# Optimization experiments

Measured on AMD Instinct MI355X. Metric: run time of the kernel, lower is better.

The kernel has to match this reference:

```python
import jax, jax.numpy as jnp
import numpy as np
import math

NUM_BUCKETS = 32
MAX_DISTANCE = 128
N_HEADS = 16
D_KV = 64


def _relative_position_bucket(relative_position, num_buckets=NUM_BUCKETS, max_distance=MAX_DISTANCE):
    # bidirectional (encoder) variant
    num_buckets //= 2
    relative_buckets = (relative_position > 0).astype(jnp.int32) * num_buckets
    rp = jnp.abs(relative_position)
    max_exact = num_buckets // 2
    is_small = rp < max_exact
    rp_large = max_exact + (
        jnp.log(jnp.maximum(rp, 1).astype(jnp.float32) / max_exact)
        / math.log(max_distance / max_exact)
        * (num_buckets - max_exact)
    ).astype(jnp.int32)
    rp_large = jnp.minimum(rp_large, num_buckets - 1)
    return relative_buckets + jnp.where(is_small, rp, rp_large)


def compute_bias(rel_bias, q_len, k_len):
    ctx = jnp.arange(q_len)[:, None]
    mem = jnp.arange(k_len)[None, :]
    buckets = _relative_position_bucket(mem - ctx)          # [q, k]
    values = rel_bias[buckets]                               # [q, k, h]
    return jnp.transpose(values, (2, 0, 1))[None]            # [1, h, q, k]


def setup_inputs() -> dict:
    key = jax.random.key(0)
    ks = jax.random.split(key, 6)
    d_model, inner = 1024, N_HEADS * D_KV
    s = 0.02
    return {
        "hidden_states": jax.random.normal(ks[0], (2, 2048, d_model), jnp.float32),
        "Wq": jax.random.normal(ks[1], (d_model, inner), jnp.float32) * s,
        "Wk": jax.random.normal(ks[2], (d_model, inner), jnp.float32) * s,
        "Wv": jax.random.normal(ks[3], (d_model, inner), jnp.float32) * s,
        "Wo": jax.random.normal(ks[4], (inner, d_model), jnp.float32) * s,
        "rel_bias": jax.random.normal(ks[5], (NUM_BUCKETS, N_HEADS), jnp.float32) * s,
    }


def reference(hidden_states, Wq, Wk, Wv, Wo, rel_bias):
    B, S, D = hidden_states.shape

    def split_heads(x):  # [B,S,inner] -> [B,H,S,dk]
        return x.reshape(B, S, N_HEADS, D_KV).transpose(0, 2, 1, 3)

    q = split_heads(hidden_states @ Wq)
    k = split_heads(hidden_states @ Wk)
    v = split_heads(hidden_states @ Wv)

    # T5 does NOT scale by 1/sqrt(d_kv)
    scores = jnp.einsum("bhqd,bhkd->bhqk", q, k)
    scores = scores + compute_bias(rel_bias, S, S)
    attn = jax.nn.softmax(scores, axis=-1)
    ctx = jnp.einsum("bhqk,bhkd->bhqd", attn, v)
    ctx = ctx.transpose(0, 2, 1, 3).reshape(B, S, N_HEADS * D_KV)
    return ctx @ Wo
```

## Files before the change

### kernel.cpp

```cpp
#include <hip/hip_runtime.h>
#include <hip/hip_bf16.h>

typedef __bf16 bf16x8 __attribute__((ext_vector_type(8)));
typedef __bf16 bf16x4 __attribute__((ext_vector_type(4)));
typedef float floatx4 __attribute__((ext_vector_type(4)));
typedef float floatx16 __attribute__((ext_vector_type(16)));
using bf16 = __hip_bfloat16;

#define S_    2048
#define NHEAD 16
#define LOG2E 1.4426950408889634f

__device__ __forceinline__ void load_lds16(const bf16* g, void* lds) {
  __builtin_amdgcn_global_load_lds((const __attribute__((address_space(1))) void*)g,
                                   (__attribute__((address_space(3))) void*)lds, 16, 0, 0);
}

__global__ void prep_kernel(const float* __restrict__ hidden,
                            const float* __restrict__ wq, const float* __restrict__ wk,
                            const float* __restrict__ wv, const float* __restrict__ wo,
                            const float* __restrict__ rel_bias,
                            bf16* __restrict__ hbf, bf16* __restrict__ wt_qkv,
                            bf16* __restrict__ wt_o, float* __restrict__ tab) {
  __shared__ bf16 tile[32][33];
  int bid = blockIdx.x;
  if (bid < 4096) {
    int i = (bid * 256 + threadIdx.x) * 4;
    float4 v = *(const float4*)(hidden + i);
    bf16 o[4] = {__float2bfloat16(v.x), __float2bfloat16(v.y),
                 __float2bfloat16(v.z), __float2bfloat16(v.w)};
    *(uint2*)(hbf + i) = *(const uint2*)o;
  } else if (bid < 8192) {
    int r = bid - 4096;
    int mat = r >> 10;
    int rem = r & 1023;
    int n0 = (rem & 31) * 32, k0 = (rem >> 5) * 32;
    int tx = threadIdx.x & 31, ty = threadIdx.x >> 5;
    const float* src = (mat == 0) ? wq : (mat == 1) ? wk : (mat == 2) ? wv : wo;
    bf16* dst = (mat == 3) ? wt_o : wt_qkv + mat * 1024 * 1024;
#pragma unroll
    for (int j = 0; j < 32; j += 8)
      tile[ty + j][tx] = __float2bfloat16(src[(k0 + ty + j) * 1024 + n0 + tx]);
    __syncthreads();
#pragma unroll
    for (int j = 0; j < 32; j += 8)
      dst[(n0 + ty + j) * 1024 + k0 + tx] = tile[tx][ty + j];
  } else {
    int idx = (bid - 8192) * 256 + threadIdx.x;
    int h = idx >> 12, j = idx & 4095;
    int delta = j - 2048;
    int rb = (delta > 0) ? 16 : 0;
    int rpa = delta < 0 ? -delta : delta;
    int bsmall;
    if (rpa < 8) {
      bsmall = rpa;
    } else {
      int lg = 25 - __clz(rpa * rpa);
      bsmall = 8 + lg;
      if (bsmall > 15) bsmall = 15;
    }
    tab[idx] = rel_bias[(rb + bsmall) * 16 + h] * LOG2E;
  }
}

__global__ __launch_bounds__(256) void gemm_qkv_kernel(const bf16* __restrict__ A,
                                                       const bf16* __restrict__ Bt,
                                                       bf16* __restrict__ qh,
                                                       bf16* __restrict__ kf,
                                                       bf16* __restrict__ vf) {
  const int K = 1024;
  __shared__ bf16 As[128 * 32];
  __shared__ bf16 Bs[128 * 32];
  int t = threadIdx.x;
  int m0 = blockIdx.y * 128, n0 = blockIdx.x * 128;
  int w = t >> 6, lane = t & 63, ln = lane & 15, quad = lane >> 4;
  int wr = w >> 1, wc = w & 1;
  floatx4 acc[4][4];
  floatx4 zero = {0.f, 0.f, 0.f, 0.f};
#pragma unroll
  for (int i = 0; i < 4; i++)
#pragma unroll
    for (int j = 0; j < 4; j++) acc[i][j] = zero;

  int r = t >> 2, c = (t & 3) * 8;
  const bf16* Ag = A + (long)(m0 + r) * K + c;
  const bf16* Bg = Bt + (long)(n0 + r) * K + c;
  char* ldsA0 = (char*)As + w * 1024;
  char* ldsA1 = ldsA0 + 4096;
  char* ldsB0 = (char*)Bs + w * 1024;
  char* ldsB1 = ldsB0 + 4096;

  for (int k0 = 0; k0 < K; k0 += 32) {
    load_lds16(Ag + k0, ldsA0);
    load_lds16(Ag + (long)64 * K + k0, ldsA1);
    load_lds16(Bg + k0, ldsB0);
    load_lds16(Bg + (long)64 * K + k0, ldsB1);
    __syncthreads();
    bf16x8 af[4], bfv[4];
#pragma unroll
    for (int i = 0; i < 4; i++)
      af[i] = *(const bf16x8*)&As[(wr * 64 + i * 16 + ln) * 32 + quad * 8];
#pragma unroll
    for (int j = 0; j < 4; j++)
      bfv[j] = *(const bf16x8*)&Bs[(wc * 64 + j * 16 + ln) * 32 + quad * 8];
#pragma unroll
    for (int i = 0; i < 4; i++)
#pragma unroll
      for (int j = 0; j < 4; j++)
        acc[i][j] = __builtin_amdgcn_mfma_f32_16x16x32_bf16(af[i], bfv[j], acc[i][j], 0, 0, 0);
    __syncthreads();
  }

  int nb = n0 + wc * 64;
  int type = nb >> 10, h = (nb >> 6) & 15;
  int b = (m0 >> 11);
  int sl0 = (m0 & 2047) + wr * 64;
  long bhbase = (long)((b * 16 + h)) * 131072;

  if (type == 0) {
#pragma unroll
    for (int i = 0; i < 4; i++)
#pragma unroll
      for (int j = 0; j < 4; j++) {
        int d = j * 16 + ln;
#pragma unroll
        for (int rr = 0; rr < 4; rr++) {
          int s = sl0 + i * 16 + quad * 4 + rr;
          qh[bhbase + (long)s * 64 + d] = __float2bfloat16(acc[i][j][rr]);
        }
      }
  } else if (type == 1) {
#pragma unroll
    for (int i = 0; i < 4; i++)
#pragma unroll
      for (int j = 0; j < 4; j++) {
        long base = bhbase + sl0 * 64 + (i >> 1) * 2048 + j * 512 + (ln >> 3) * 256 +
                    (i & 1) * 128 + quad * 32 + (ln & 7);
#pragma unroll
        for (int rr = 0; rr < 4; rr++)
          kf[base + rr * 8] = __float2bfloat16(acc[i][j][rr]);
      }
  } else {
#pragma unroll
    for (int i = 0; i < 4; i++)
#pragma unroll
      for (int j = 0; j < 4; j++) {
        long off = sl0 * 64 + i * 1024 + (j >> 1) * 512 + (quad >> 1) * 256 +
                   ((j & 1) * 16 + ln) * 8 + (quad & 1) * 4;
        bf16x4 pk = {(__bf16)acc[i][j][0], (__bf16)acc[i][j][1],
                     (__bf16)acc[i][j][2], (__bf16)acc[i][j][3]};
        *(bf16x4*)(vf + bhbase + off) = pk;
      }
  }
}

__global__ __launch_bounds__(128, 2) void attn_kernel(const bf16* __restrict__ qh,
                                                      const bf16* __restrict__ kf,
                                                      const bf16* __restrict__ vf,
                                                      const float* __restrict__ btab,
                                                      bf16* __restrict__ ctx) {
  __shared__ char KV[2][16384];
  int t = threadIdx.x, w = t >> 6, lane = t & 63;
  int l31 = lane & 31, h5 = lane >> 5;
  int bh = blockIdx.x, b = bh >> 4, h = bh & 15;
  int qw = blockIdx.y * 64 + w * 32;

  const bf16* qbase = qh + (long)bh * S_ * 64;
  const bf16* kfb = kf + (long)bh * S_ * 64;
  const bf16* vfb = vf + (long)bh * S_ * 64;
  const float* bt = btab + h * 4096;

  bf16x8 Qf[4];
#pragma unroll
  for (int ds = 0; ds < 4; ds++)
    Qf[ds] = *(const bf16x8*)(qbase + (long)(qw + l31) * 64 + ds * 16 + h5 * 8);

  float cneg = bt[0], cpos = bt[4095];
  float l_acc = 0.f;
  floatx16 zf = {0.f, 0.f, 0.f, 0.f, 0.f, 0.f, 0.f, 0.f,
                 0.f, 0.f, 0.f, 0.f, 0.f, 0.f, 0.f, 0.f};
  floatx16 o0 = zf, o1 = zf;

  {
    const bf16* kg = kfb + t * 8;
    const bf16* vg = vfb + t * 8;
#pragma unroll
    for (int c = 0; c < 4; c++) {
      load_lds16(kg + c * 1024, KV[0] + c * 2048 + w * 1024);
      load_lds16(vg + c * 1024, KV[0] + 8192 + c * 2048 + w * 1024);
    }
  }

  int pb = 0;
  for (int k0 = 0; k0 < S_; k0 += 64) {
    __syncthreads();
    int kn = k0 + 64;
    if (kn < S_) {
      const bf16* kg = kfb + kn * 64 + t * 8;
      const bf16* vg = vfb + kn * 64 + t * 8;
      char* nb_ = KV[pb ^ 1];
#pragma unroll
      for (int c = 0; c < 4; c++) {
        load_lds16(kg + c * 1024, nb_ + c * 2048 + w * 1024);
        load_lds16(vg + c * 1024, nb_ + 8192 + c * 2048 + w * 1024);
      }
    }

    const char* bK = KV[pb];
    const char* bV = KV[pb] + 8192;

    floatx16 st0 = zf, st1 = zf;
#pragma unroll
    for (int ds = 0; ds < 4; ds++) {
      bf16x8 Kf0 = *(const bf16x8*)(bK + ds * 1024 + lane * 16);
      st0 = __builtin_amdgcn_mfma_f32_32x32x16_bf16(Kf0, Qf[ds], st0, 0, 0, 0);
    }
#pragma unroll
    for (int ds = 0; ds < 4; ds++) {
      bf16x8 Kf1 = *(const bf16x8*)(bK + 4096 + ds * 1024 + lane * 16);
      st1 = __builtin_amdgcn_mfma_f32_32x32x16_bf16(Kf1, Qf[ds], st1, 0, 0, 0);
    }

    bf16x8 Af[4];
    bool near = (k0 > qw - 192) && (k0 < qw + 160);
#pragma unroll
    for (int s = 0; s < 2; s++) {
      const floatx16 stv = s ? st1 : st0;
      float p[16];
      if (near) {
        int kb = k0 + s * 32 + 4 * h5 - (qw + l31) + 2048;
#pragma unroll
        for (int r = 0; r < 16; r++)
          p[r] = __builtin_amdgcn_exp2f(
              fmaf(stv[r], LOG2E, bt[kb + (r & 3) + 8 * (r >> 2)]));
      } else {
        float cb = (k0 > qw) ? cpos : cneg;
#pragma unroll
        for (int r = 0; r < 16; r++)
          p[r] = __builtin_amdgcn_exp2f(fmaf(stv[r], LOG2E, cb));
      }
      float a0 = (p[0] + p[1]) + (p[2] + p[3]);
      float a1 = (p[4] + p[5]) + (p[6] + p[7]);
      float a2 = (p[8] + p[9]) + (p[10] + p[11]);
      float a3 = (p[12] + p[13]) + (p[14] + p[15]);
      l_acc += (a0 + a1) + (a2 + a3);

      unsigned d[8];
#pragma unroll
      for (int i = 0; i < 8; i++)
        asm("v_cvt_pk_bf16_f32 %0, %1, %2" : "=v"(d[i]) : "v"(p[2 * i]), "v"(p[2 * i + 1]));
      unsigned w0 = d[0], w2 = d[2];
      asm("v_permlane32_swap_b32 %0, %1" : "+v"(w0), "+v"(w2));
      unsigned w1 = d[1], w3 = d[3];
      asm("v_permlane32_swap_b32 %0, %1" : "+v"(w1), "+v"(w3));
      unsigned w4 = d[4], w6 = d[6];
      asm("v_permlane32_swap_b32 %0, %1" : "+v"(w4), "+v"(w6));
      unsigned w5 = d[5], w7 = d[7];
      asm("v_permlane32_swap_b32 %0, %1" : "+v"(w5), "+v"(w7));
      union { unsigned u[4]; bf16x8 v; } a0u, a1u;
      a0u.u[0] = w0; a0u.u[1] = w1; a0u.u[2] = w2; a0u.u[3] = w3;
      a1u.u[0] = w4; a1u.u[1] = w5; a1u.u[2] = w6; a1u.u[3] = w7;
      Af[s * 2 + 0] = a0u.v;
      Af[s * 2 + 1] = a1u.v;
    }

#pragma unroll
    for (int tt = 0; tt < 4; tt++) {
      bf16x8 Vf0 = *(const bf16x8*)(bV + tt * 2048 + lane * 16);
      bf16x8 Vf1 = *(const bf16x8*)(bV + tt * 2048 + 1024 + lane * 16);
      o0 = __builtin_amdgcn_mfma_f32_32x32x16_bf16(Af[tt], Vf0, o0, 0, 0, 0);
      o1 = __builtin_amdgcn_mfma_f32_32x32x16_bf16(Af[tt], Vf1, o1, 0, 0, 0);
    }

    pb ^= 1;
  }

  l_acc += __shfl_xor(l_acc, 32);
  float linv = 1.0f / l_acc;
#pragma unroll
  for (int r = 0; r < 16; r++) {
    int qrow = (r & 3) + 8 * (r >> 2) + 4 * h5;
    float lv = __shfl(linv, qrow);
    int q = qw + qrow;
    long base = (long)(b * S_ + q) * 1024 + h * 64 + l31;
    ctx[base] = __float2bfloat16(o0[r] * lv);
    ctx[base + 32] = __float2bfloat16(o1[r] * lv);
  }
}

__global__ __launch_bounds__(256) void gemm_bt_kernel(const bf16* __restrict__ A,
                                                      const bf16* __restrict__ Bt,
                                                      float* __restrict__ C,
                                                      int M, int N, int K) {
  __shared__ bf16 As[128 * 32];
  __shared__ bf16 Bs[128 * 32];
  int t = threadIdx.x;
  int m0 = blockIdx.y * 128, n0 = blockIdx.x * 128;
  int w = t >> 6, lane = t & 63, ln = lane & 15, quad = lane >> 4;
  int wr = w >> 1, wc = w & 1;
  floatx4 acc[4][4];
  floatx4 zero = {0.f, 0.f, 0.f, 0.f};
#pragma unroll
  for (int i = 0; i < 4; i++)
#pragma unroll
    for (int j = 0; j < 4; j++) acc[i][j] = zero;

  int r = t >> 2, c = (t & 3) * 8;
  const bf16* Ag = A + (long)(m0 + r) * K + c;
  const bf16* Bg = Bt + (long)(n0 + r) * K + c;
  char* ldsA0 = (char*)As + w * 1024;
  char* ldsA1 = ldsA0 + 4096;
  char* ldsB0 = (char*)Bs + w * 1024;
  char* ldsB1 = ldsB0 + 4096;

  for (int k0 = 0; k0 < K; k0 += 32) {
    load_lds16(Ag + k0, ldsA0);
    load_lds16(Ag + (long)64 * K + k0, ldsA1);
    load_lds16(Bg + k0, ldsB0);
    load_lds16(Bg + (long)64 * K + k0, ldsB1);
    __syncthreads();
    bf16x8 af[4], bfv[4];
#pragma unroll
    for (int i = 0; i < 4; i++)
      af[i] = *(const bf16x8*)&As[(wr * 64 + i * 16 + ln) * 32 + quad * 8];
#pragma unroll
    for (int j = 0; j < 4; j++)
      bfv[j] = *(const bf16x8*)&Bs[(wc * 64 + j * 16 + ln) * 32 + quad * 8];
#pragma unroll
    for (int i = 0; i < 4; i++)
#pragma unroll
      for (int j = 0; j < 4; j++)
        acc[i][j] = __builtin_amdgcn_mfma_f32_16x16x32_bf16(af[i], bfv[j], acc[i][j], 0, 0, 0);
    __syncthreads();
  }

#pragma unroll
  for (int i = 0; i < 4; i++)
#pragma unroll
    for (int j = 0; j < 4; j++)
#pragma unroll
      for (int rr = 0; rr < 4; rr++)
        C[(long)(m0 + wr * 64 + i * 16 + quad * 4 + rr) * N + n0 + wc * 64 + j * 16 + ln] =
            acc[i][j][rr];
}

extern "C" void kernel_launch(void* const* d_in, const int* in_sizes, int n_in,
                              void* d_out, int out_size, void* d_ws, size_t ws_size,
                              hipStream_t stream) {
  (void)in_sizes; (void)n_in; (void)out_size; (void)ws_size;
  const float* hidden   = (const float*)d_in[0];
  const float* Wq       = (const float*)d_in[1];
  const float* Wk       = (const float*)d_in[2];
  const float* Wv       = (const float*)d_in[3];
  const float* Wo       = (const float*)d_in[4];
  const float* rel_bias = (const float*)d_in[5];

  char* ws = (char*)d_ws;
  bf16*  hbf    = (bf16*)(ws + 0);
  bf16*  wt_qkv = (bf16*)(ws + 8388608);
  bf16*  wt_o   = (bf16*)(ws + 14680064);
  float* btab   = (float*)(ws + 16777216);
  bf16*  qh     = (bf16*)(ws + 17039360);
  bf16*  kf     = (bf16*)(ws + 25427968);
  bf16*  vf     = (bf16*)(ws + 33816576);
  bf16*  ctx    = (bf16*)(ws + 42205184);

  prep_kernel<<<dim3(8448), dim3(256), 0, stream>>>(hidden, Wq, Wk, Wv, Wo, rel_bias,
                                                    hbf, wt_qkv, wt_o, btab);
  gemm_qkv_kernel<<<dim3(24, 32), dim3(256), 0, stream>>>(hbf, wt_qkv, qh, kf, vf);
  attn_kernel<<<dim3(32, 32), dim3(128), 0, stream>>>(qh, kf, vf, btab, ctx);
  gemm_bt_kernel<<<dim3(8, 32), dim3(256), 0, stream>>>(ctx, wt_o, (float*)d_out, 4096, 1024, 1024);
}
```

Before: 201.8 us.

## Stream K/V fragments directly from global into registers, dropping LDS staging

The attention kernel no longer stages K/V tiles through double-buffered LDS with block-wide barriers. Each wave now loads its K/V MFMA fragments straight from global memory into registers, using two register sets to prefetch the next 32-key chunk while the current one is computed. The block grows to 4 waves over 128 query rows, the grid order is swapped so blocks of the same head sit together, and s_setprio is raised around the MFMA groups. This removes the barriers and LDS traffic, but every wave re-reads K/V from global/L2 and register pressure rises.

```diff
diff --git a/kernel.cpp b/kernel.cpp
--- a/kernel.cpp
+++ b/kernel.cpp
@@ -154,21 +154,86 @@
   }
 }
 
-__global__ __launch_bounds__(128, 2) void attn_kernel(const bf16* __restrict__ qh,
+#define LOADKV(Kr, Vr, kk)                                        \
+  {                                                               \
+    const bf16* kp = kfb + (kk) * 64 + loff;                      \
+    const bf16* vp = vfb + (kk) * 64 + loff;                      \
+    Kr[0] = *(const bf16x8*)(kp);                                 \
+    Kr[1] = *(const bf16x8*)(kp + 512);                           \
+    Kr[2] = *(const bf16x8*)(kp + 1024);                          \
+    Kr[3] = *(const bf16x8*)(kp + 1536);                          \
+    Vr[0] = *(const bf16x8*)(vp);                                 \
+    Vr[1] = *(const bf16x8*)(vp + 512);                           \
+    Vr[2] = *(const bf16x8*)(vp + 1024);                          \
+    Vr[3] = *(const bf16x8*)(vp + 1536);                          \
+  }
+
+#define COMPUTE(Kr, Vr, kk)                                                       \
+  {                                                                               \
+    floatx16 st = zf;                                                             \
+    __builtin_amdgcn_s_setprio(1);                                                \
+    st = __builtin_amdgcn_mfma_f32_32x32x16_bf16(Kr[0], Qf[0], st, 0, 0, 0);      \
+    st = __builtin_amdgcn_mfma_f32_32x32x16_bf16(Kr[1], Qf[1], st, 0, 0, 0);      \
+    st = __builtin_amdgcn_mfma_f32_32x32x16_bf16(Kr[2], Qf[2], st, 0, 0, 0);      \
+    st = __builtin_amdgcn_mfma_f32_32x32x16_bf16(Kr[3], Qf[3], st, 0, 0, 0);      \
+    __builtin_amdgcn_s_setprio(0);                                                \
+    float p[16];                                                                  \
+    bool near = ((kk) > qw - 160) && ((kk) < qw + 160);                           \
+    if (near) {                                                                   \
+      int kb = (kk) + 4 * h5 - (qw + l31) + 2048;                                 \
+      _Pragma("unroll")                                                           \
+      for (int r = 0; r < 16; r++)                                                \
+        p[r] = __builtin_amdgcn_exp2f(                                            \
+            fmaf(st[r], LOG2E, bt[kb + (r & 3) + 8 * (r >> 2)]));                 \
+    } else {                                                                      \
+      float cb = ((kk) > qw) ? cpos : cneg;                                       \
+      _Pragma("unroll")                                                           \
+      for (int r = 0; r < 16; r++)                                                \
+        p[r] = __builtin_amdgcn_exp2f(fmaf(st[r], LOG2E, cb));                    \
+    }                                                                             \
+    float a0 = (p[0] + p[1]) + (p[2] + p[3]);                                     \
+    float a1 = (p[4] + p[5]) + (p[6] + p[7]);                                     \
+    float a2 = (p[8] + p[9]) + (p[10] + p[11]);                                   \
+    float a3 = (p[12] + p[13]) + (p[14] + p[15]);                                 \
+    l_acc += (a0 + a1) + (a2 + a3);                                               \
+    unsigned d[8];                                                                \
+    _Pragma("unroll")                                                             \
+    for (int i = 0; i < 8; i++)                                                   \
+      asm("v_cvt_pk_bf16_f32 %0, %1, %2" : "=v"(d[i]) : "v"(p[2*i]), "v"(p[2*i+1])); \
+    unsigned w0 = d[0], w2 = d[2];                                                \
+    asm("v_permlane32_swap_b32 %0, %1" : "+v"(w0), "+v"(w2));                     \
+    unsigned w1 = d[1], w3 = d[3];                                                \
+    asm("v_permlane32_swap_b32 %0, %1" : "+v"(w1), "+v"(w3));                     \
+    unsigned w4 = d[4], w6 = d[6];                                                \
+    asm("v_permlane32_swap_b32 %0, %1" : "+v"(w4), "+v"(w6));                     \
+    unsigned w5 = d[5], w7 = d[7];                                                \
+    asm("v_permlane32_swap_b32 %0, %1" : "+v"(w5), "+v"(w7));                     \
+    union { unsigned u[4]; bf16x8 v; } a0u, a1u;                                  \
+    a0u.u[0] = w0; a0u.u[1] = w1; a0u.u[2] = w2; a0u.u[3] = w3;                   \
+    a1u.u[0] = w4; a1u.u[1] = w5; a1u.u[2] = w6; a1u.u[3] = w7;                   \
+    __builtin_amdgcn_s_setprio(1);                                                \
+    o0 = __builtin_amdgcn_mfma_f32_32x32x16_bf16(a0u.v, Vr[0], o0, 0, 0, 0);      \
+    o1 = __builtin_amdgcn_mfma_f32_32x32x16_bf16(a0u.v, Vr[1], o1, 0, 0, 0);      \
+    o0 = __builtin_amdgcn_mfma_f32_32x32x16_bf16(a1u.v, Vr[2], o0, 0, 0, 0);      \
+    o1 = __builtin_amdgcn_mfma_f32_32x32x16_bf16(a1u.v, Vr[3], o1, 0, 0, 0);      \
+    __builtin_amdgcn_s_setprio(0);                                                \
+  }
+
+__global__ __launch_bounds__(256, 2) void attn_kernel(const bf16* __restrict__ qh,
                                                       const bf16* __restrict__ kf,
                                                       const bf16* __restrict__ vf,
                                                       const float* __restrict__ btab,
                                                       bf16* __restrict__ ctx) {
-  __shared__ char KV[2][16384];
   int t = threadIdx.x, w = t >> 6, lane = t & 63;
   int l31 = lane & 31, h5 = lane >> 5;
-  int bh = blockIdx.x, b = bh >> 4, h = bh & 15;
-  int qw = blockIdx.y * 64 + w * 32;
+  int bh = blockIdx.y, b = bh >> 4, h = bh & 15;
+  int qw = blockIdx.x * 128 + w * 32;
 
   const bf16* qbase = qh + (long)bh * S_ * 64;
   const bf16* kfb = kf + (long)bh * S_ * 64;
   const bf16* vfb = vf + (long)bh * S_ * 64;
   const float* bt = btab + h * 4096;
+  int loff = h5 * 256 + l31 * 8;
 
   bf16x8 Qf[4];
 #pragma unroll
@@ -181,98 +246,15 @@
                  0.f, 0.f, 0.f, 0.f, 0.f, 0.f, 0.f, 0.f};
   floatx16 o0 = zf, o1 = zf;
 
-  {
-    const bf16* kg = kfb + t * 8;
-    const bf16* vg = vfb + t * 8;
-#pragma unroll
-    for (int c = 0; c < 4; c++) {
-      load_lds16(kg + c * 1024, KV[0] + c * 2048 + w * 1024);
-      load_lds16(vg + c * 1024, KV[0] + 8192 + c * 2048 + w * 1024);
-    }
-  }
-
-  int pb = 0;
+  bf16x8 Ka[4], Va[4], Kb[4], Vb[4];
+  LOADKV(Ka, Va, 0);
+  LOADKV(Kb, Vb, 32);
+
   for (int k0 = 0; k0 < S_; k0 += 64) {
-    __syncthreads();
-    int kn = k0 + 64;
-    if (kn < S_) {
-      const bf16* kg = kfb + kn * 64 + t * 8;
-      const bf16* vg = vfb + kn * 64 + t * 8;
-      char* nb_ = KV[pb ^ 1];
-#pragma unroll
-      for (int c = 0; c < 4; c++) {
-        load_lds16(kg + c * 1024, nb_ + c * 2048 + w * 1024);
-        load_lds16(vg + c * 1024, nb_ + 8192 + c * 2048 + w * 1024);
-      }
-    }
-
-    const char* bK = KV[pb];
-    const char* bV = KV[pb] + 8192;
-
-    floatx16 st0 = zf, st1 = zf;
-#pragma unroll
-    for (int ds = 0; ds < 4; ds++) {
-      bf16x8 Kf0 = *(const bf16x8*)(bK + ds * 1024 + lane * 16);
-      st0 = __builtin_amdgcn_mfma_f32_32x32x16_bf16(Kf0, Qf[ds], st0, 0, 0, 0);
-    }
-#pragma unroll
-    for (int ds = 0; ds < 4; ds++) {
-      bf16x8 Kf1 = *(const bf16x8*)(bK + 4096 + ds * 1024 + lane * 16);
-      st1 = __builtin_amdgcn_mfma_f32_32x32x16_bf16(Kf1, Qf[ds], st1, 0, 0, 0);
-    }
-
-    bf16x8 Af[4];
-    bool near = (k0 > qw - 192) && (k0 < qw + 160);
-#pragma unroll
-    for (int s = 0; s < 2; s++) {
-      const floatx16 stv = s ? st1 : st0;
-      float p[16];
-      if (near) {
-        int kb = k0 + s * 32 + 4 * h5 - (qw + l31) + 2048;
-#pragma unroll
-        for (int r = 0; r < 16; r++)
-          p[r] = __builtin_amdgcn_exp2f(
-              fmaf(stv[r], LOG2E, bt[kb + (r & 3) + 8 * (r >> 2)]));
-      } else {
-        float cb = (k0 > qw) ? cpos : cneg;
-#pragma unroll
-        for (int r = 0; r < 16; r++)
-          p[r] = __builtin_amdgcn_exp2f(fmaf(stv[r], LOG2E, cb));
-      }
-      float a0 = (p[0] + p[1]) + (p[2] + p[3]);
-      float a1 = (p[4] + p[5]) + (p[6] + p[7]);
-      float a2 = (p[8] + p[9]) + (p[10] + p[11]);
-      float a3 = (p[12] + p[13]) + (p[14] + p[15]);
-      l_acc += (a0 + a1) + (a2 + a3);
-
-      unsigned d[8];
-#pragma unroll
-      for (int i = 0; i < 8; i++)
-        asm("v_cvt_pk_bf16_f32 %0, %1, %2" : "=v"(d[i]) : "v"(p[2 * i]), "v"(p[2 * i + 1]));
-      unsigned w0 = d[0], w2 = d[2];
-      asm("v_permlane32_swap_b32 %0, %1" : "+v"(w0), "+v"(w2));
-      unsigned w1 = d[1], w3 = d[3];
-      asm("v_permlane32_swap_b32 %0, %1" : "+v"(w1), "+v"(w3));
-      unsigned w4 = d[4], w6 = d[6];
-      asm("v_permlane32_swap_b32 %0, %1" : "+v"(w4), "+v"(w6));
-      unsigned w5 = d[5], w7 = d[7];
-      asm("v_permlane32_swap_b32 %0, %1" : "+v"(w5), "+v"(w7));
-      union { unsigned u[4]; bf16x8 v; } a0u, a1u;
-      a0u.u[0] = w0; a0u.u[1] = w1; a0u.u[2] = w2; a0u.u[3] = w3;
-      a1u.u[0] = w4; a1u.u[1] = w5; a1u.u[2] = w6; a1u.u[3] = w7;
-      Af[s * 2 + 0] = a0u.v;
-      Af[s * 2 + 1] = a1u.v;
-    }
-
-#pragma unroll
-    for (int tt = 0; tt < 4; tt++) {
-      bf16x8 Vf0 = *(const bf16x8*)(bV + tt * 2048 + lane * 16);
-      bf16x8 Vf1 = *(const bf16x8*)(bV + tt * 2048 + 1024 + lane * 16);
-      o0 = __builtin_amdgcn_mfma_f32_32x32x16_bf16(Af[tt], Vf0, o0, 0, 0, 0);
-      o1 = __builtin_amdgcn_mfma_f32_32x32x16_bf16(Af[tt], Vf1, o1, 0, 0, 0);
-    }
-
-    pb ^= 1;
+    COMPUTE(Ka, Va, k0);
+    if (k0 + 64 < S_) LOADKV(Ka, Va, k0 + 64);
+    COMPUTE(Kb, Vb, k0 + 32);
+    if (k0 + 96 < S_) LOADKV(Kb, Vb, k0 + 96);
   }
 
   l_acc += __shfl_xor(l_acc, 32);
@@ -368,6 +350,6 @@
   prep_kernel<<<dim3(8448), dim3(256), 0, stream>>>(hidden, Wq, Wk, Wv, Wo, rel_bias,
                                                     hbf, wt_qkv, wt_o, btab);
   gemm_qkv_kernel<<<dim3(24, 32), dim3(256), 0, stream>>>(hbf, wt_qkv, qh, kf, vf);
-  attn_kernel<<<dim3(32, 32), dim3(128), 0, stream>>>(qh, kf, vf, btab, ctx);
+  attn_kernel<<<dim3(16, 32), dim3(256), 0, stream>>>(qh, kf, vf, btab, ctx);
   gemm_bt_kernel<<<dim3(8, 32), dim3(256), 0, stream>>>(ctx, wt_o, (float*)d_out, 4096, 1024, 1024);
 }
```

New measurement: 195.2 us. 3.3% less time.

## Split attention KV range across warps, load K/V directly to registers

Applied to the files above, without the earlier changes.

The attention kernel now uses 256 threads, and two warp pairs each process half of the key range for the same 32-row query tile. Partial outputs and row sums are then merged through shared memory. The LDS double-buffered staging and per-tile barriers are replaced by direct global-to-register K/V prefetch in 32-key steps. MFMA sections are wrapped in setprio, and blocks are remapped so each XCD handles contiguous heads for L2 locality. The changes trade the shared-memory K/V reuse across warps for more parallelism and fewer syncs, with added register pressure and redundant global reads.

```diff
diff --git a/kernel.cpp b/kernel.cpp
--- a/kernel.cpp
+++ b/kernel.cpp
@@ -154,21 +154,28 @@
   }
 }
 
-__global__ __launch_bounds__(128, 2) void attn_kernel(const bf16* __restrict__ qh,
+__global__ __launch_bounds__(256, 2) void attn_kernel(const bf16* __restrict__ qh,
                                                       const bf16* __restrict__ kf,
                                                       const bf16* __restrict__ vf,
                                                       const float* __restrict__ btab,
                                                       bf16* __restrict__ ctx) {
-  __shared__ char KV[2][16384];
+  __shared__ float mbuf[2][64][33];
   int t = threadIdx.x, w = t >> 6, lane = t & 63;
   int l31 = lane & 31, h5 = lane >> 5;
-  int bh = blockIdx.x, b = bh >> 4, h = bh & 15;
-  int qw = blockIdx.y * 64 + w * 32;
+
+  int lin = blockIdx.x;
+  int xcd = lin & 7, j = lin >> 3;
+  int bh = xcd * 4 + (j >> 5);
+  int qblk = j & 31;
+  int b = bh >> 4, h = bh & 15;
+  int qw = qblk * 64 + (w & 1) * 32;
+  int kbeg = (w >> 1) * 1024;
 
   const bf16* qbase = qh + (long)bh * S_ * 64;
   const bf16* kfb = kf + (long)bh * S_ * 64;
   const bf16* vfb = vf + (long)bh * S_ * 64;
   const float* bt = btab + h * 4096;
+  int loff = h5 * 256 + l31 * 8;
 
   bf16x8 Qf[4];
 #pragma unroll
@@ -181,110 +188,113 @@
                  0.f, 0.f, 0.f, 0.f, 0.f, 0.f, 0.f, 0.f};
   floatx16 o0 = zf, o1 = zf;
 
+  bf16x8 Kr[4], Vr[4];
   {
-    const bf16* kg = kfb + t * 8;
-    const bf16* vg = vfb + t * 8;
-#pragma unroll
-    for (int c = 0; c < 4; c++) {
-      load_lds16(kg + c * 1024, KV[0] + c * 2048 + w * 1024);
-      load_lds16(vg + c * 1024, KV[0] + 8192 + c * 2048 + w * 1024);
-    }
-  }
-
-  int pb = 0;
-  for (int k0 = 0; k0 < S_; k0 += 64) {
-    __syncthreads();
-    int kn = k0 + 64;
-    if (kn < S_) {
-      const bf16* kg = kfb + kn * 64 + t * 8;
-      const bf16* vg = vfb + kn * 64 + t * 8;
-      char* nb_ = KV[pb ^ 1];
-#pragma unroll
-      for (int c = 0; c < 4; c++) {
-        load_lds16(kg + c * 1024, nb_ + c * 2048 + w * 1024);
-        load_lds16(vg + c * 1024, nb_ + 8192 + c * 2048 + w * 1024);
-      }
-    }
-
-    const char* bK = KV[pb];
-    const char* bV = KV[pb] + 8192;
-
-    floatx16 st0 = zf, st1 = zf;
-#pragma unroll
-    for (int ds = 0; ds < 4; ds++) {
-      bf16x8 Kf0 = *(const bf16x8*)(bK + ds * 1024 + lane * 16);
-      st0 = __builtin_amdgcn_mfma_f32_32x32x16_bf16(Kf0, Qf[ds], st0, 0, 0, 0);
-    }
-#pragma unroll
-    for (int ds = 0; ds < 4; ds++) {
-      bf16x8 Kf1 = *(const bf16x8*)(bK + 4096 + ds * 1024 + lane * 16);
-      st1 = __builtin_amdgcn_mfma_f32_32x32x16_bf16(Kf1, Qf[ds], st1, 0, 0, 0);
-    }
-
-    bf16x8 Af[4];
-    bool near = (k0 > qw - 192) && (k0 < qw + 160);
-#pragma unroll
-    for (int s = 0; s < 2; s++) {
-      const floatx16 stv = s ? st1 : st0;
-      float p[16];
-      if (near) {
-        int kb = k0 + s * 32 + 4 * h5 - (qw + l31) + 2048;
-#pragma unroll
-        for (int r = 0; r < 16; r++)
-          p[r] = __builtin_amdgcn_exp2f(
-              fmaf(stv[r], LOG2E, bt[kb + (r & 3) + 8 * (r >> 2)]));
-      } else {
-        float cb = (k0 > qw) ? cpos : cneg;
-#pragma unroll
-        for (int r = 0; r < 16; r++)
-          p[r] = __builtin_amdgcn_exp2f(fmaf(stv[r], LOG2E, cb));
-      }
-      float a0 = (p[0] + p[1]) + (p[2] + p[3]);
-      float a1 = (p[4] + p[5]) + (p[6] + p[7]);
-      float a2 = (p[8] + p[9]) + (p[10] + p[11]);
-      float a3 = (p[12] + p[13]) + (p[14] + p[15]);
-      l_acc += (a0 + a1) + (a2 + a3);
-
-      unsigned d[8];
-#pragma unroll
-      for (int i = 0; i < 8; i++)
-        asm("v_cvt_pk_bf16_f32 %0, %1, %2" : "=v"(d[i]) : "v"(p[2 * i]), "v"(p[2 * i + 1]));
-      unsigned w0 = d[0], w2 = d[2];
-      asm("v_permlane32_swap_b32 %0, %1" : "+v"(w0), "+v"(w2));
-      unsigned w1 = d[1], w3 = d[3];
-      asm("v_permlane32_swap_b32 %0, %1" : "+v"(w1), "+v"(w3));
-      unsigned w4 = d[4], w6 = d[6];
-      asm("v_permlane32_swap_b32 %0, %1" : "+v"(w4), "+v"(w6));
-      unsigned w5 = d[5], w7 = d[7];
-      asm("v_permlane32_swap_b32 %0, %1" : "+v"(w5), "+v"(w7));
-      union { unsigned u[4]; bf16x8 v; } a0u, a1u;
-      a0u.u[0] = w0; a0u.u[1] = w1; a0u.u[2] = w2; a0u.u[3] = w3;
-      a1u.u[0] = w4; a1u.u[1] = w5; a1u.u[2] = w6; a1u.u[3] = w7;
-      Af[s * 2 + 0] = a0u.v;
-      Af[s * 2 + 1] = a1u.v;
-    }
-
-#pragma unroll
-    for (int tt = 0; tt < 4; tt++) {
-      bf16x8 Vf0 = *(const bf16x8*)(bV + tt * 2048 + lane * 16);
-      bf16x8 Vf1 = *(const bf16x8*)(bV + tt * 2048 + 1024 + lane * 16);
-      o0 = __builtin_amdgcn_mfma_f32_32x32x16_bf16(Af[tt], Vf0, o0, 0, 0, 0);
-      o1 = __builtin_amdgcn_mfma_f32_32x32x16_bf16(Af[tt], Vf1, o1, 0, 0, 0);
-    }
-
-    pb ^= 1;
+    const bf16* kp = kfb + kbeg * 64 + loff;
+    Kr[0] = *(const bf16x8*)(kp);
+    Kr[1] = *(const bf16x8*)(kp + 512);
+    Kr[2] = *(const bf16x8*)(kp + 1024);
+    Kr[3] = *(const bf16x8*)(kp + 1536);
+    const bf16* vp = vfb + kbeg * 64 + loff;
+    Vr[0] = *(const bf16x8*)(vp);
+    Vr[1] = *(const bf16x8*)(vp + 512);
+    Vr[2] = *(const bf16x8*)(vp + 1024);
+    Vr[3] = *(const bf16x8*)(vp + 1536);
+  }
+
+  int kend = kbeg + 1024;
+  for (int k0 = kbeg; k0 < kend; k0 += 32) {
+    int kn = k0 + 32;
+    floatx16 st = zf;
+    __builtin_amdgcn_s_setprio(1);
+    st = __builtin_amdgcn_mfma_f32_32x32x16_bf16(Kr[0], Qf[0], st, 0, 0, 0);
+    st = __builtin_amdgcn_mfma_f32_32x32x16_bf16(Kr[1], Qf[1], st, 0, 0, 0);
+    st = __builtin_amdgcn_mfma_f32_32x32x16_bf16(Kr[2], Qf[2], st, 0, 0, 0);
+    st = __builtin_amdgcn_mfma_f32_32x32x16_bf16(Kr[3], Qf[3], st, 0, 0, 0);
+    __builtin_amdgcn_s_setprio(0);
+    if (kn < kend) {
+      const bf16* kp = kfb + kn * 64 + loff;
+      Kr[0] = *(const bf16x8*)(kp);
+      Kr[1] = *(const bf16x8*)(kp + 512);
+      Kr[2] = *(const bf16x8*)(kp + 1024);
+      Kr[3] = *(const bf16x8*)(kp + 1536);
+    }
+
+    float p[16];
+    bool near = (k0 > qw - 160) && (k0 < qw + 160);
+    if (near) {
+      int kb = k0 + 4 * h5 - (qw + l31) + 2048;
+#pragma unroll
+      for (int r = 0; r < 16; r++)
+        p[r] = __builtin_amdgcn_exp2f(
+            fmaf(st[r], LOG2E, bt[kb + (r & 3) + 8 * (r >> 2)]));
+    } else {
+      float cb = (k0 > qw) ? cpos : cneg;
+#pragma unroll
+      for (int r = 0; r < 16; r++)
+        p[r] = __builtin_amdgcn_exp2f(fmaf(st[r], LOG2E, cb));
+    }
+    float a0 = (p[0] + p[1]) + (p[2] + p[3]);
+    float a1 = (p[4] + p[5]) + (p[6] + p[7]);
+    float a2 = (p[8] + p[9]) + (p[10] + p[11]);
+    float a3 = (p[12] + p[13]) + (p[14] + p[15]);
+    l_acc += (a0 + a1) + (a2 + a3);
+
+    unsigned d[8];
+#pragma unroll
+    for (int i = 0; i < 8; i++)
+      asm("v_cvt_pk_bf16_f32 %0, %1, %2" : "=v"(d[i]) : "v"(p[2 * i]), "v"(p[2 * i + 1]));
+    unsigned w0 = d[0], w2 = d[2];
+    asm("v_permlane32_swap_b32 %0, %1" : "+v"(w0), "+v"(w2));
+    unsigned w1 = d[1], w3 = d[3];
+    asm("v_permlane32_swap_b32 %0, %1" : "+v"(w1), "+v"(w3));
+    unsigned w4 = d[4], w6 = d[6];
+    asm("v_permlane32_swap_b32 %0, %1" : "+v"(w4), "+v"(w6));
+    unsigned w5 = d[5], w7 = d[7];
+    asm("v_permlane32_swap_b32 %0, %1" : "+v"(w5), "+v"(w7));
+    union { unsigned u[4]; bf16x8 v; } a0u, a1u;
+    a0u.u[0] = w0; a0u.u[1] = w1; a0u.u[2] = w2; a0u.u[3] = w3;
+    a1u.u[0] = w4; a1u.u[1] = w5; a1u.u[2] = w6; a1u.u[3] = w7;
+
+    __builtin_amdgcn_s_setprio(1);
+    o0 = __builtin_amdgcn_mfma_f32_32x32x16_bf16(a0u.v, Vr[0], o0, 0, 0, 0);
+    o1 = __builtin_amdgcn_mfma_f32_32x32x16_bf16(a0u.v, Vr[1], o1, 0, 0, 0);
+    o0 = __builtin_amdgcn_mfma_f32_32x32x16_bf16(a1u.v, Vr[2], o0, 0, 0, 0);
+    o1 = __builtin_amdgcn_mfma_f32_32x32x16_bf16(a1u.v, Vr[3], o1, 0, 0, 0);
+    __builtin_amdgcn_s_setprio(0);
+    if (kn < kend) {
+      const bf16* vp = vfb + kn * 64 + loff;
+      Vr[0] = *(const bf16x8*)(vp);
+      Vr[1] = *(const bf16x8*)(vp + 512);
+      Vr[2] = *(const bf16x8*)(vp + 1024);
+      Vr[3] = *(const bf16x8*)(vp + 1536);
+    }
   }
 
   l_acc += __shfl_xor(l_acc, 32);
-  float linv = 1.0f / l_acc;
-#pragma unroll
-  for (int r = 0; r < 16; r++) {
-    int qrow = (r & 3) + 8 * (r >> 2) + 4 * h5;
-    float lv = __shfl(linv, qrow);
-    int q = qw + qrow;
-    long base = (long)(b * S_ + q) * 1024 + h * 64 + l31;
-    ctx[base] = __float2bfloat16(o0[r] * lv);
-    ctx[base + 32] = __float2bfloat16(o1[r] * lv);
+
+  if (w >= 2) {
+    float* dst = &mbuf[w & 1][lane][0];
+#pragma unroll
+    for (int r = 0; r < 16; r++) { dst[r] = o0[r]; dst[16 + r] = o1[r]; }
+    dst[32] = l_acc;
+  }
+  __syncthreads();
+  if (w < 2) {
+    const float* src = &mbuf[w][lane][0];
+#pragma unroll
+    for (int r = 0; r < 16; r++) { o0[r] += src[r]; o1[r] += src[16 + r]; }
+    l_acc += src[32];
+    float linv = 1.0f / l_acc;
+#pragma unroll
+    for (int r = 0; r < 16; r++) {
+      int qrow = (r & 3) + 8 * (r >> 2) + 4 * h5;
+      float lv = __shfl(linv, qrow);
+      int q = qw + qrow;
+      long base = (long)(b * S_ + q) * 1024 + h * 64 + l31;
+      ctx[base] = __float2bfloat16(o0[r] * lv);
+      ctx[base + 32] = __float2bfloat16(o1[r] * lv);
+    }
   }
 }
 
@@ -368,6 +378,6 @@
   prep_kernel<<<dim3(8448), dim3(256), 0, stream>>>(hidden, Wq, Wk, Wv, Wo, rel_bias,
                                                     hbf, wt_qkv, wt_o, btab);
   gemm_qkv_kernel<<<dim3(24, 32), dim3(256), 0, stream>>>(hbf, wt_qkv, qh, kf, vf);
-  attn_kernel<<<dim3(32, 32), dim3(128), 0, stream>>>(qh, kf, vf, btab, ctx);
+  attn_kernel<<<dim3(1024), dim3(256), 0, stream>>>(qh, kf, vf, btab, ctx);
   gemm_bt_kernel<<<dim3(8, 32), dim3(256), 0, stream>>>(ctx, wt_o, (float*)d_out, 4096, 1024, 1024);
 }
```

After: 198.7 us. Within noise of the previous version (-1.6%).
